# Kernel tuning notes

Measured on AMD Instinct MI355X. Metric: run time of the kernel, lower is better.

The kernel has to match this reference:

```python
import jax, jax.numpy as jnp
import numpy as np

EMBED_DIM = 768
NUM_HEADS = 12
HEAD_DIM = EMBED_DIM // NUM_HEADS


def setup_inputs() -> dict:
    key = jax.random.key(0)
    k_x, k_wqkv, k_bqkv, k_wp, k_bp = jax.random.split(key, 5)
    B, N, C = 2, 2048, EMBED_DIM
    lim_qkv = 1.0 / np.sqrt(C)
    lim_p = 1.0 / np.sqrt(C)
    return {
        "x": jax.random.normal(k_x, (B, N, C), dtype=jnp.float32),
        # torch Linear weights: [out_features, in_features]
        "w_qkv": jax.random.uniform(k_wqkv, (3 * C, C), minval=-lim_qkv, maxval=lim_qkv, dtype=jnp.float32),
        "b_qkv": jax.random.uniform(k_bqkv, (3 * C,), minval=-lim_qkv, maxval=lim_qkv, dtype=jnp.float32),
        "w_proj": jax.random.uniform(k_wp, (C, C), minval=-lim_p, maxval=lim_p, dtype=jnp.float32),
        "b_proj": jax.random.uniform(k_bp, (C,), minval=-lim_p, maxval=lim_p, dtype=jnp.float32),
    }


def reference(x, w_qkv, b_qkv, w_proj, b_proj):
    b, n, c = x.shape
    h, d = NUM_HEADS, HEAD_DIM
    qkv = x @ w_qkv.T + b_qkv                      # [b, n, 3c]
    qkv = qkv.reshape(b, n, 3, h, d).transpose(2, 0, 3, 1, 4)  # [3, b, h, n, d]
    q, k, v = qkv[0], qkv[1], qkv[2]
    scale = d ** -0.5
    attn = jnp.einsum('bhnd,bhmd->bhnm', q, k) * scale  # [b, h, n, n]
    attn = jax.nn.softmax(attn, axis=-1)
    # dropout is identity at inference (eval mode)
    out = jnp.einsum('bhnm,bhmd->bhnd', attn, v)        # [b, h, n, d]
    out = out.transpose(0, 2, 1, 3).reshape(b, n, c)    # [b, n, c]
    return out @ w_proj.T + b_proj
```

## Files before the change

kernel.cpp:

```cpp
#include <hip/hip_runtime.h>
#include <cstdint>
#include <cstddef>

using u16    = uint16_t;
using u16x4  = __attribute__((ext_vector_type(4))) uint16_t;
using u16x8  = __attribute__((ext_vector_type(8))) uint16_t;
using bf16x8 = __attribute__((ext_vector_type(8))) __bf16;
using f32x4  = __attribute__((ext_vector_type(4))) float;

__device__ __forceinline__ u16 f2b(float f) {
    union { float f; uint32_t u; } x; x.f = f;
    uint32_t r = x.u + 0x7FFFu + ((x.u >> 16) & 1u);
    return (u16)(r >> 16);
}
__device__ __forceinline__ uint32_t pk2(float a, float b) {
    return (uint32_t)f2b(a) | ((uint32_t)f2b(b) << 16);
}
__device__ __forceinline__ bf16x8 ld8(const u16* p) {
    union { u16x8 v; u16x4 h[2]; } r;
    r.h[0] = *(const u16x4*)p;
    r.h[1] = *(const u16x4*)(p + 4);
    return __builtin_bit_cast(bf16x8, r.v);
}
__device__ __forceinline__ void st8(u16* p, u16x8 v) {
    union { u16x8 v; u16x4 h[2]; } r; r.v = v;
    *(u16x4*)p       = r.h[0];
    *(u16x4*)(p + 4) = r.h[1];
}

__device__ __forceinline__ void load16_async(const u16* g, u16* lds_base) {
    __builtin_amdgcn_global_load_lds(
        (const __attribute__((address_space(1))) u16*)g,
        (__attribute__((address_space(3))) u16*)(uint32_t)(uintptr_t)lds_base,
        16, 0, 0);
}

__global__ void conv_k(const float* __restrict__ x,  u16* __restrict__ xb,  int nx4,
                       const float* __restrict__ w1, u16* __restrict__ w1b, int n14,
                       const float* __restrict__ w2, u16* __restrict__ w2b, int n24)
{
    const int t   = blockIdx.x * blockDim.x + threadIdx.x;
    const int stp = gridDim.x * blockDim.x;
    for (int i = t; i < nx4; i += stp) {
        f32x4 v = ((const f32x4*)x)[i];
        u16x4 o;
        #pragma unroll
        for (int e = 0; e < 4; e++) o[e] = f2b(v[e]);
        ((u16x4*)xb)[i] = o;
    }
    for (int i = t; i < n14; i += stp) {
        f32x4 v = ((const f32x4*)w1)[i];
        u16x4 o;
        #pragma unroll
        for (int e = 0; e < 4; e++) o[e] = f2b(v[e]);
        ((u16x4*)w1b)[i] = o;
    }
    for (int i = t; i < n24; i += stp) {
        f32x4 v = ((const f32x4*)w2)[i];
        u16x4 o;
        #pragma unroll
        for (int e = 0; e < 4; e++) o[e] = f2b(v[e]);
        ((u16x4*)w2b)[i] = o;
    }
}

__global__ __launch_bounds__(256, 2) void gemm_qkv(
    const u16* __restrict__ A, const u16* __restrict__ W,
    const float* __restrict__ bias,
    u16* __restrict__ O0, u16* __restrict__ O1, u16* __restrict__ O2)
{
    __shared__ alignas(16) u16 As[128 * 32];
    __shared__ alignas(16) u16 Bs[128 * 32];
    const int tid  = threadIdx.x;
    const int wid  = tid >> 6, lane = tid & 63;
    const int quad = lane >> 4, lc = lane & 15;
    const int row0 = blockIdx.x * 128, col0 = blockIdx.y * 128;
    const int wm   = (wid >> 1) * 64, wn = (wid & 1) * 64;

    const int srA = wid * 32 + (lane >> 2);
    const int scA = (lane & 3) * 8;

    f32x4 acc[4][4] = {};

    for (int k0 = 0; k0 < 768; k0 += 32) {
        __syncthreads();
        #pragma unroll
        for (int t = 0; t < 2; t++) {
            load16_async(&A[(row0 + srA + t*16) * 768 + k0 + scA], &As[wid*1024 + t*512]);
            load16_async(&W[(col0 + srA + t*16) * 768 + k0 + scA], &Bs[wid*1024 + t*512]);
        }
        __syncthreads();

        bf16x8 a[4], b[4];
        #pragma unroll
        for (int i = 0; i < 4; i++)
            a[i] = __builtin_bit_cast(bf16x8, *(const u16x8*)&As[(wm + i*16 + lc)*32 + quad*8]);
        #pragma unroll
        for (int j = 0; j < 4; j++)
            b[j] = __builtin_bit_cast(bf16x8, *(const u16x8*)&Bs[(wn + j*16 + lc)*32 + quad*8]);
        #pragma unroll
        for (int i = 0; i < 4; i++)
            #pragma unroll
            for (int j = 0; j < 4; j++)
                acc[i][j] = __builtin_amdgcn_mfma_f32_16x16x32_bf16(a[i], b[j], acc[i][j], 0, 0, 0);
    }

    #pragma unroll
    for (int i = 0; i < 4; i++) {
        #pragma unroll
        for (int j = 0; j < 4; j++) {
            const int gc = col0 + wn + j*16 + lc;
            const float bv = bias[gc];
            #pragma unroll
            for (int r = 0; r < 4; r++) {
                const int gr = row0 + wm + i*16 + quad*4 + r;
                const u16 ob = f2b(acc[i][j][r] + bv);
                const int which = gc / 768;
                const int c2 = gc - which * 768;
                if (which == 0)      O0[gr * 768 + c2] = ob;
                else if (which == 1) O1[gr * 768 + c2] = ob;
                else {
                    const int hh = c2 >> 6, dd = c2 & 63;
                    const int bb = gr >> 11, nn = gr & 2047;
                    O2[((bb*12 + hh)*64 + dd)*2048 + nn] = ob;
                }
            }
        }
    }
}

__global__ __launch_bounds__(256, 4) void gemm_proj(
    const u16* __restrict__ A, const u16* __restrict__ W,
    const float* __restrict__ bias, float* __restrict__ F0)
{
    __shared__ alignas(16) u16 As[64 * 32];
    __shared__ alignas(16) u16 Bs[64 * 32];
    const int tid  = threadIdx.x;
    const int wid  = tid >> 6, lane = tid & 63;
    const int quad = lane >> 4, lc = lane & 15;
    const int row0 = blockIdx.x * 64, col0 = blockIdx.y * 64;
    const int wm   = (wid >> 1) * 32, wn = (wid & 1) * 32;

    const int srA = wid * 16 + (lane >> 2);
    const int scA = (lane & 3) * 8;

    f32x4 acc[2][2] = {};

    for (int k0 = 0; k0 < 768; k0 += 32) {
        __syncthreads();
        load16_async(&A[(row0 + srA) * 768 + k0 + scA], &As[wid*512]);
        load16_async(&W[(col0 + srA) * 768 + k0 + scA], &Bs[wid*512]);
        __syncthreads();

        bf16x8 a[2], b[2];
        #pragma unroll
        for (int i = 0; i < 2; i++)
            a[i] = __builtin_bit_cast(bf16x8, *(const u16x8*)&As[(wm + i*16 + lc)*32 + quad*8]);
        #pragma unroll
        for (int j = 0; j < 2; j++)
            b[j] = __builtin_bit_cast(bf16x8, *(const u16x8*)&Bs[(wn + j*16 + lc)*32 + quad*8]);
        #pragma unroll
        for (int i = 0; i < 2; i++)
            #pragma unroll
            for (int j = 0; j < 2; j++)
                acc[i][j] = __builtin_amdgcn_mfma_f32_16x16x32_bf16(a[i], b[j], acc[i][j], 0, 0, 0);
    }

    #pragma unroll
    for (int i = 0; i < 2; i++)
        #pragma unroll
        for (int j = 0; j < 2; j++) {
            const int gc = col0 + wn + j*16 + lc;
            const float bv = bias[gc];
            #pragma unroll
            for (int r = 0; r < 4; r++) {
                const int gr = row0 + wm + i*16 + quad*4 + r;
                F0[gr * 768 + gc] = acc[i][j][r] + bv;
            }
        }
}

__global__ __launch_bounds__(256, 3) void attn_k(
    const u16* __restrict__ Q, const u16* __restrict__ K,
    const u16* __restrict__ V, u16* __restrict__ O)
{
    __shared__ u16 Ks[128][68];
    __shared__ u16 Vs[64][140];
    __shared__ alignas(16) u16 Ps[4][16][76];

    const int tid  = threadIdx.x;
    const int wid  = tid >> 6, lane = tid & 63;
    const int quad = lane >> 4, lc = lane & 15;
    const int li = blockIdx.x;
    const int bh = li >> 5, qt = li & 31;
    const int b = bh / 12, h = bh - b * 12;
    const int q0 = qt * 64 + wid * 16;

    const u16* Qp = Q + ((size_t)b * 2048) * 768 + h * 64;
    const u16* Kp = K + ((size_t)b * 2048) * 768 + h * 64;
    const u16* Vp = V + (size_t)bh * 64 * 2048;
    u16*       Op = O + ((size_t)b * 2048) * 768 + h * 64;

    bf16x8 qf[2];
    #pragma unroll
    for (int kb = 0; kb < 2; kb++) {
        u16x8 t = *(const u16x8*)&Qp[(q0 + lc) * 768 + kb*32 + quad*8];
        u16x8 sc;
        #pragma unroll
        for (int e = 0; e < 8; e++) {
            union { uint32_t u; float f; } z; z.u = ((uint32_t)t[e]) << 16;
            sc[e] = f2b(z.f * 0.125f);
        }
        qf[kb] = __builtin_bit_cast(bf16x8, sc);
    }

    float l_ = 0.f;
    f32x4 o_[4] = {};

    const int kr = tid >> 3, kseg = (tid & 7) * 8;
    const int vr = tid >> 4, vseg = (tid & 15) * 8;

    u16x8 kpre[4], vpre[4];
    #pragma unroll
    for (int p = 0; p < 4; p++)
        kpre[p] = *(const u16x8*)&Kp[(kr + p*32)*768 + kseg];
    #pragma unroll
    for (int p = 0; p < 4; p++)
        vpre[p] = *(const u16x8*)&Vp[(vr + p*16)*2048 + vseg];

    for (int kt = 0; kt < 16; kt++) {
        __syncthreads();
        #pragma unroll
        for (int p = 0; p < 4; p++)
            st8(&Ks[kr + p*32][kseg], kpre[p]);
        #pragma unroll
        for (int p = 0; p < 4; p++)
            st8(&Vs[vr + p*16][vseg], vpre[p]);
        __syncthreads();

        if (kt < 15) {
            #pragma unroll
            for (int p = 0; p < 4; p++)
                kpre[p] = *(const u16x8*)&Kp[((kt+1)*128 + kr + p*32)*768 + kseg];
            #pragma unroll
            for (int p = 0; p < 4; p++)
                vpre[p] = *(const u16x8*)&Vp[(vr + p*16)*2048 + (kt+1)*128 + vseg];
        }

        f32x4 s[8] = {};
        #pragma unroll
        for (int nb = 0; nb < 8; nb++) {
            bf16x8 k0f = ld8(&Ks[nb*16 + lc][quad*8]);
            bf16x8 k1f = ld8(&Ks[nb*16 + lc][32 + quad*8]);
            s[nb] = __builtin_amdgcn_mfma_f32_16x16x32_bf16(k0f, qf[0], s[nb], 0, 0, 0);
            s[nb] = __builtin_amdgcn_mfma_f32_16x16x32_bf16(k1f, qf[1], s[nb], 0, 0, 0);
        }

        float acc = 0.f;
        #pragma unroll
        for (int nb = 0; nb < 8; nb++)
            #pragma unroll
            for (int r = 0; r < 4; r++) {
                float p = __expf(s[nb][r]);
                s[nb][r] = p;
                acc += p;
            }
        l_ += acc;

        #pragma unroll
        for (int hf = 0; hf < 2; hf++) {
            #pragma unroll
            for (int nb4 = 0; nb4 < 4; nb4++) {
                const int nb = hf*4 + nb4;
                uint2 w;
                w.x = pk2(s[nb][0], s[nb][1]);
                w.y = pk2(s[nb][2], s[nb][3]);
                *(uint2*)&Ps[wid][lc][nb4*16 + quad*4] = w;
            }
            #pragma unroll
            for (int c = 0; c < 2; c++) {
                bf16x8 pf = ld8(&Ps[wid][lc][c*32 + quad*8]);
                #pragma unroll
                for (int db = 0; db < 4; db++) {
                    bf16x8 vf = ld8(&Vs[db*16 + lc][hf*64 + c*32 + quad*8]);
                    o_[db] = __builtin_amdgcn_mfma_f32_16x16x32_bf16(vf, pf, o_[db], 0, 0, 0);
                }
            }
        }
    }

    l_ += __shfl_xor(l_, 16);
    l_ += __shfl_xor(l_, 32);
    const float rinv = 1.0f / l_;

    #pragma unroll
    for (int db = 0; db < 4; db++) {
        u16x4 o;
        #pragma unroll
        for (int r = 0; r < 4; r++) o[r] = f2b(o_[db][r] * rinv);
        *(u16x4*)&Op[(size_t)(q0 + lc) * 768 + db*16 + quad*4] = o;
    }
}

extern "C" void kernel_launch(void* const* d_in, const int* in_sizes, int n_in,
                              void* d_out, int out_size, void* d_ws, size_t ws_size,
                              hipStream_t stream)
{
    const float* x    = (const float*)d_in[0];
    const float* wqkv = (const float*)d_in[1];
    const float* bqkv = (const float*)d_in[2];
    const float* wp   = (const float*)d_in[3];
    const float* bp   = (const float*)d_in[4];
    float* out = (float*)d_out;
    char* ws = (char*)d_ws;

    u16* Qw    = (u16*)(ws);
    u16* Vt    = (u16*)(ws + 6291456);
    u16* wqkvb = (u16*)(ws + 12582912);
    u16* wpb   = (u16*)(ws + 16121856);
    u16* Kw    = (u16*)d_out;
    u16* xb    = (u16*)((char*)d_out + 6291456);

    conv_k<<<512, 256, 0, stream>>>(x, xb, 3145728/4, wqkv, wqkvb, 1769472/4, wp, wpb, 589824/4);
    gemm_qkv<<<dim3(32, 18), 256, 0, stream>>>(xb, wqkvb, bqkv, Qw, Kw, Vt);
    attn_k<<<768, 256, 0, stream>>>(Qw, Kw, Vt, Qw);
    gemm_proj<<<dim3(64, 12), 256, 0, stream>>>(Qw, wpb, bp, out);
}
```

Before: 168.6 us.

## Split attention key tiles across waves and reduce partial outputs in LDS

The attention kernel now has each wave handle all 64 queries of the block against its own 32-key slice of every 128-key tile, instead of 16 queries against all keys. Each K/V fragment read from LDS is reused across four query groups, but each wave now holds 16 output accumulators. The partial outputs and row sums are then reduced across waves through LDS at the end. Occupancy is lowered to 2 blocks per SM to fit the extra registers, and the bf16 packing uses the native conversion instead of manual rounding.

```diff
diff --git a/kernel.cpp b/kernel.cpp
--- a/kernel.cpp
+++ b/kernel.cpp
@@ -5,6 +5,7 @@
 using u16    = uint16_t;
 using u16x4  = __attribute__((ext_vector_type(4))) uint16_t;
 using u16x8  = __attribute__((ext_vector_type(8))) uint16_t;
+using bf16x2 = __attribute__((ext_vector_type(2))) __bf16;
 using bf16x8 = __attribute__((ext_vector_type(8))) __bf16;
 using f32x4  = __attribute__((ext_vector_type(4))) float;
 
@@ -14,7 +15,8 @@
     return (u16)(r >> 16);
 }
 __device__ __forceinline__ uint32_t pk2(float a, float b) {
-    return (uint32_t)f2b(a) | ((uint32_t)f2b(b) << 16);
+    bf16x2 t; t[0] = (__bf16)a; t[1] = (__bf16)b;
+    return __builtin_bit_cast(uint32_t, t);
 }
 __device__ __forceinline__ bf16x8 ld8(const u16* p) {
     union { u16x8 v; u16x4 h[2]; } r;
@@ -180,13 +182,16 @@
         }
 }
 
-__global__ __launch_bounds__(256, 3) void attn_k(
+__global__ __launch_bounds__(256, 2) void attn_k(
     const u16* __restrict__ Q, const u16* __restrict__ K,
     const u16* __restrict__ V, u16* __restrict__ O)
 {
-    __shared__ u16 Ks[128][68];
-    __shared__ u16 Vs[64][140];
-    __shared__ alignas(16) u16 Ps[4][16][76];
+    __shared__ alignas(16) char lds[53760];
+    u16* Ks = (u16*)(lds);
+    u16* Vs = (u16*)(lds + 17408);
+    u16* Ps = (u16*)(lds + 35328);
+    float* Obuf = (float*)(lds);
+    float* Lbuf = (float*)(lds + 35328);
 
     const int tid  = threadIdx.x;
     const int wid  = tid >> 6, lane = tid & 63;
@@ -194,31 +199,34 @@
     const int li = blockIdx.x;
     const int bh = li >> 5, qt = li & 31;
     const int b = bh / 12, h = bh - b * 12;
-    const int q0 = qt * 64 + wid * 16;
+    const int q0 = qt * 64;
 
     const u16* Qp = Q + ((size_t)b * 2048) * 768 + h * 64;
     const u16* Kp = K + ((size_t)b * 2048) * 768 + h * 64;
     const u16* Vp = V + (size_t)bh * 64 * 2048;
     u16*       Op = O + ((size_t)b * 2048) * 768 + h * 64;
 
-    bf16x8 qf[2];
-    #pragma unroll
-    for (int kb = 0; kb < 2; kb++) {
-        u16x8 t = *(const u16x8*)&Qp[(q0 + lc) * 768 + kb*32 + quad*8];
-        u16x8 sc;
-        #pragma unroll
-        for (int e = 0; e < 8; e++) {
-            union { uint32_t u; float f; } z; z.u = ((uint32_t)t[e]) << 16;
-            sc[e] = f2b(z.f * 0.125f);
-        }
-        qf[kb] = __builtin_bit_cast(bf16x8, sc);
-    }
-
-    float l_ = 0.f;
-    f32x4 o_[4] = {};
+    bf16x8 qf[4][2];
+    #pragma unroll
+    for (int qg = 0; qg < 4; qg++)
+        #pragma unroll
+        for (int kb = 0; kb < 2; kb++) {
+            u16x8 t = *(const u16x8*)&Qp[(q0 + qg*16 + lc) * 768 + kb*32 + quad*8];
+            bf16x8 sc;
+            #pragma unroll
+            for (int e = 0; e < 8; e++) {
+                union { uint32_t u; float f; } z; z.u = ((uint32_t)t[e]) << 16;
+                sc[e] = (__bf16)(z.f * 0.125f);
+            }
+            qf[qg][kb] = sc;
+        }
+
+    float l_[4] = {};
+    f32x4 o_[4][4] = {};
 
     const int kr = tid >> 3, kseg = (tid & 7) * 8;
     const int vr = tid >> 4, vseg = (tid & 15) * 8;
+    const int kb0 = wid * 32;
 
     u16x8 kpre[4], vpre[4];
     #pragma unroll
@@ -232,10 +240,10 @@
         __syncthreads();
         #pragma unroll
         for (int p = 0; p < 4; p++)
-            st8(&Ks[kr + p*32][kseg], kpre[p]);
+            st8(&Ks[(kr + p*32)*68 + kseg], kpre[p]);
         #pragma unroll
         for (int p = 0; p < 4; p++)
-            st8(&Vs[vr + p*16][vseg], vpre[p]);
+            st8(&Vs[(vr + p*16)*140 + vseg], vpre[p]);
         __syncthreads();
 
         if (kt < 15) {
@@ -247,58 +255,91 @@
                 vpre[p] = *(const u16x8*)&Vp[(vr + p*16)*2048 + (kt+1)*128 + vseg];
         }
 
-        f32x4 s[8] = {};
-        #pragma unroll
-        for (int nb = 0; nb < 8; nb++) {
-            bf16x8 k0f = ld8(&Ks[nb*16 + lc][quad*8]);
-            bf16x8 k1f = ld8(&Ks[nb*16 + lc][32 + quad*8]);
-            s[nb] = __builtin_amdgcn_mfma_f32_16x16x32_bf16(k0f, qf[0], s[nb], 0, 0, 0);
-            s[nb] = __builtin_amdgcn_mfma_f32_16x16x32_bf16(k1f, qf[1], s[nb], 0, 0, 0);
-        }
-
-        float acc = 0.f;
-        #pragma unroll
-        for (int nb = 0; nb < 8; nb++)
-            #pragma unroll
-            for (int r = 0; r < 4; r++) {
-                float p = __expf(s[nb][r]);
-                s[nb][r] = p;
-                acc += p;
-            }
-        l_ += acc;
-
-        #pragma unroll
-        for (int hf = 0; hf < 2; hf++) {
-            #pragma unroll
-            for (int nb4 = 0; nb4 < 4; nb4++) {
-                const int nb = hf*4 + nb4;
+        f32x4 s[2][4] = {};
+        #pragma unroll
+        for (int g = 0; g < 2; g++) {
+            bf16x8 k0f = ld8(&Ks[(kb0 + g*16 + lc)*68 + quad*8]);
+            bf16x8 k1f = ld8(&Ks[(kb0 + g*16 + lc)*68 + 32 + quad*8]);
+            #pragma unroll
+            for (int qg = 0; qg < 4; qg++) {
+                s[g][qg] = __builtin_amdgcn_mfma_f32_16x16x32_bf16(k0f, qf[qg][0], s[g][qg], 0, 0, 0);
+                s[g][qg] = __builtin_amdgcn_mfma_f32_16x16x32_bf16(k1f, qf[qg][1], s[g][qg], 0, 0, 0);
+            }
+        }
+
+        #pragma unroll
+        for (int g = 0; g < 2; g++)
+            #pragma unroll
+            for (int qg = 0; qg < 4; qg++)
+                #pragma unroll
+                for (int r = 0; r < 4; r++) {
+                    float p = __expf(s[g][qg][r]);
+                    s[g][qg][r] = p;
+                    l_[qg] += p;
+                }
+
+        #pragma unroll
+        for (int g = 0; g < 2; g++)
+            #pragma unroll
+            for (int qg = 0; qg < 4; qg++) {
                 uint2 w;
-                w.x = pk2(s[nb][0], s[nb][1]);
-                w.y = pk2(s[nb][2], s[nb][3]);
-                *(uint2*)&Ps[wid][lc][nb4*16 + quad*4] = w;
-            }
-            #pragma unroll
-            for (int c = 0; c < 2; c++) {
-                bf16x8 pf = ld8(&Ps[wid][lc][c*32 + quad*8]);
+                w.x = pk2(s[g][qg][0], s[g][qg][1]);
+                w.y = pk2(s[g][qg][2], s[g][qg][3]);
+                *(uint2*)&Ps[(wid*64 + qg*16 + lc)*36 + g*16 + quad*4] = w;
+            }
+
+        bf16x8 pf[4], vf[4];
+        #pragma unroll
+        for (int qg = 0; qg < 4; qg++)
+            pf[qg] = ld8(&Ps[(wid*64 + qg*16 + lc)*36 + quad*8]);
+        #pragma unroll
+        for (int dg = 0; dg < 4; dg++)
+            vf[dg] = ld8(&Vs[(dg*16 + lc)*140 + kb0 + quad*8]);
+        #pragma unroll
+        for (int dg = 0; dg < 4; dg++)
+            #pragma unroll
+            for (int qg = 0; qg < 4; qg++)
+                o_[dg][qg] = __builtin_amdgcn_mfma_f32_16x16x32_bf16(vf[dg], pf[qg], o_[dg][qg], 0, 0, 0);
+    }
+
+    #pragma unroll
+    for (int qg = 0; qg < 4; qg++) {
+        l_[qg] += __shfl_xor(l_[qg], 16);
+        l_[qg] += __shfl_xor(l_[qg], 32);
+    }
+    __syncthreads();
+    if (quad == 0)
+        #pragma unroll
+        for (int qg = 0; qg < 4; qg++)
+            Lbuf[wid*64 + qg*16 + lc] = l_[qg];
+    __syncthreads();
+
+    const int eq = tid & 63;
+    const int ed = (tid >> 6) * 8;
+    const float linv = 1.0f / (Lbuf[0*64 + eq] + Lbuf[1*64 + eq] +
+                               Lbuf[2*64 + eq] + Lbuf[3*64 + eq]);
+
+    #pragma unroll
+    for (int dh = 0; dh < 2; dh++) {
+        __syncthreads();
+        #pragma unroll
+        for (int b2 = 0; b2 < 2; b2++) {
+            const int dg = dh*2 + b2;
+            #pragma unroll
+            for (int qg = 0; qg < 4; qg++)
                 #pragma unroll
-                for (int db = 0; db < 4; db++) {
-                    bf16x8 vf = ld8(&Vs[db*16 + lc][hf*64 + c*32 + quad*8]);
-                    o_[db] = __builtin_amdgcn_mfma_f32_16x16x32_bf16(vf, pf, o_[db], 0, 0, 0);
-                }
-            }
-        }
-    }
-
-    l_ += __shfl_xor(l_, 16);
-    l_ += __shfl_xor(l_, 32);
-    const float rinv = 1.0f / l_;
-
-    #pragma unroll
-    for (int db = 0; db < 4; db++) {
-        u16x4 o;
-        #pragma unroll
-        for (int r = 0; r < 4; r++) o[r] = f2b(o_[db][r] * rinv);
-        *(u16x4*)&Op[(size_t)(q0 + lc) * 768 + db*16 + quad*4] = o;
+                for (int r = 0; r < 4; r++)
+                    Obuf[(wid*32 + b2*16 + quad*4 + r)*64 + qg*16 + lc] = o_[dg][qg][r];
+        }
+        __syncthreads();
+        u16x8 ov;
+        #pragma unroll
+        for (int j = 0; j < 8; j++) {
+            const float sum = Obuf[(0*32 + ed + j)*64 + eq] + Obuf[(1*32 + ed + j)*64 + eq] +
+                              Obuf[(2*32 + ed + j)*64 + eq] + Obuf[(3*32 + ed + j)*64 + eq];
+            ov[j] = f2b(sum * linv);
+        }
+        *(u16x8*)&Op[(size_t)(q0 + eq) * 768 + dh*32 + ed] = ov;
     }
 }
 
```

New measurement: 166.9 us. No clear change (-1.0%).
